# Kernel tuning notes

Measured on AMD Instinct MI355X. Metric: run time of the kernel, lower is better.

## Reference

```python
import jax, jax.numpy as jnp
import numpy as np

N, E, G = 50000, 1600000, 512
H, NF_IN, NF_OUT, GF_OUT, EDIM, DEPTH = 128, 64, 64, 128, 16, 3
EPS = 1e-5


def seg_softmax(logits, seg, num):
    m = jax.ops.segment_max(logits, seg, num_segments=num)
    e = jnp.exp(logits - m[seg])
    s = jax.ops.segment_sum(e, seg, num_segments=num)
    return e / s[seg]


def batchnorm_train(x, gamma, beta):
    mu = jnp.mean(x, axis=0)
    var = jnp.mean((x - mu) ** 2, axis=0)  # biased, as torch BN training
    return (x - mu) * jax.lax.rsqrt(var + EPS) * gamma + beta


def setup_inputs() -> dict:
    key = jax.random.key(0)
    ks = jax.random.split(key, 20)
    inp = {}
    inp['x'] = jax.random.normal(ks[0], (N, NF_IN), jnp.float32)
    inp['edge_index'] = jax.random.randint(ks[1], (2, E), 0, N, jnp.int64)
    inp['edge_attr'] = jax.random.normal(ks[2], (E, EDIM), jnp.float32)
    inp['batch'] = jnp.sort(jax.random.randint(ks[3], (N,), 0, G, jnp.int64))
    inp['num_graphs'] = G
    s = 0.05
    inp['Wi'] = jax.random.normal(ks[4], (H, NF_IN), jnp.float32) * s
    inp['bi'] = jnp.zeros((H,), jnp.float32)
    inp['gat_W'] = jax.random.normal(ks[5], (DEPTH, H, 2 * H), jnp.float32) * s
    inp['gat_a'] = jax.random.normal(ks[6], (DEPTH, 2 * H), jnp.float32) * s
    inp['nfW1'] = jax.random.normal(ks[7], (H, H), jnp.float32) * s
    inp['nfb1'] = jnp.zeros((H,), jnp.float32)
    inp['nf_g'] = jnp.ones((H,), jnp.float32)
    inp['nf_b'] = jnp.zeros((H,), jnp.float32)
    inp['nfW2'] = jax.random.normal(ks[8], (NF_OUT, H), jnp.float32) * s
    inp['nfb2'] = jnp.zeros((NF_OUT,), jnp.float32)
    inp['gfW1'] = jax.random.normal(ks[9], (H, H), jnp.float32) * s
    inp['gfb1'] = jnp.zeros((H,), jnp.float32)
    inp['gf_g'] = jnp.ones((H,), jnp.float32)
    inp['gf_b'] = jnp.zeros((H,), jnp.float32)
    inp['gfW2'] = jax.random.normal(ks[10], (GF_OUT, H), jnp.float32) * s
    inp['gfb2'] = jnp.zeros((GF_OUT,), jnp.float32)
    return inp


def reference(x, edge_index, edge_attr, batch, num_graphs, Wi, bi, gat_W, gat_a,
              nfW1, nfb1, nf_g, nf_b, nfW2, nfb2,
              gfW1, gfb1, gf_g, gf_b, gfW2, gfb2):
    src, dst = edge_index[0], edge_index[1]
    nf = x @ Wi.T + bi  # [N,H]
    for i in range(DEPTH):
        src_nf = nf[src]            # [E,H]
        dst_nf = nf[dst]            # [E,H]
        ef = jnp.concatenate([src_nf, dst_nf], axis=-1) @ gat_a[i]  # [E]
        alpha = seg_softmax(ef, dst, N)
        agg = jax.ops.segment_sum(alpha[:, None] * src_nf, dst, num_segments=N)
        nf = jax.nn.relu(jnp.concatenate([nf, agg], axis=-1) @ gat_W[i].T)
    # 3-iteration attention pooling over graphs
    h = nf
    for _ in range(3):
        logits = jnp.sum(h * nf, axis=-1)  # [N]
        alpha = seg_softmax(logits, batch, num_graphs)
        h = alpha[:, None] * nf
    gf = jax.ops.segment_sum(h, batch, num_segments=num_graphs)  # [G,H]
    nf_out = jax.nn.relu(batchnorm_train(nf @ nfW1.T + nfb1, nf_g, nf_b)) @ nfW2.T + nfb2
    gf_out = jax.nn.relu(batchnorm_train(gf @ gfW1.T + gfb1, gf_g, gf_b)) @ gfW2.T + gfb2
    return nf_out, edge_attr, gf_out
```

## Files before the change

### kernel.cpp

```cpp
#include <hip/hip_runtime.h>

#define NN 50000
#define NE 1600000
#define NG 512
#define HD 128
#define NGRP 8
#define GRPSZ ((NN + NGRP - 1) / NGRP)
#define PCAP 28672

typedef __attribute__((ext_vector_type(8))) short bf16x8;
typedef __attribute__((ext_vector_type(4))) float f32x4;

static __device__ __forceinline__ unsigned bf16rn(float x) {
  unsigned b = __float_as_uint(x);
  return (b + 0x7FFFu + ((b >> 16) & 1u)) >> 16;
}
static __device__ __forceinline__ float bf16tof(unsigned short u) {
  return __uint_as_float(((unsigned)u) << 16);
}

__global__ void __launch_bounds__(256) k_part(const int* __restrict__ src,
                                              const int* __restrict__ dst,
                                              uint2* __restrict__ pairs,
                                              int* __restrict__ pcnt) {
  __shared__ uint2 buf[8][512];
  __shared__ int lcnt[8];
  __shared__ int gbase[8];
  __shared__ int nfl[8];
  const int tid = threadIdx.x;
  const int b = blockIdx.x & 7;
  if (tid < 8) lcnt[tid] = 0;
  __syncthreads();
  const int stride = gridDim.x * 256;
  for (int base_e = blockIdx.x * 256; base_e < NE; base_e += stride) {
    int e = base_e + tid;
    bool valid = e < NE;
    if (valid) {
      int d = dst[e];
      int s = src[e];
      int g = d / GRPSZ;
      int pos = atomicAdd(&lcnt[g], 1);
      buf[g][pos] = make_uint2((unsigned)d, (unsigned)s);
    }
    __syncthreads();
    if (tid < 8) {
      int c = lcnt[tid];
      int nf = (c >= 256) ? 256 : 0;
      nfl[tid] = nf;
      gbase[tid] = nf ? atomicAdd(&pcnt[tid * 8 + b], nf) : 0;
    }
    __syncthreads();
#pragma unroll
    for (int g0 = 0; g0 < 8; ++g0) {
      if (nfl[g0]) {
        int gb = gbase[g0] + tid;
        if (gb < PCAP)
          pairs[(size_t)(g0 * 8 + b) * PCAP + gb] = buf[g0][tid];
      }
    }
    __syncthreads();
#pragma unroll
    for (int g0 = 0; g0 < 8; ++g0) {
      if (nfl[g0]) {
        int rem = lcnt[g0] - 256;
        if (tid < rem) buf[g0][tid] = buf[g0][256 + tid];
      }
    }
    __syncthreads();
    if (tid < 8 && nfl[tid]) lcnt[tid] -= 256;
    __syncthreads();
  }
  if (tid < 8) {
    int c = lcnt[tid];
    gbase[tid] = c ? atomicAdd(&pcnt[tid * 8 + b], c) : 0;
  }
  __syncthreads();
#pragma unroll
  for (int g0 = 0; g0 < 8; ++g0) {
    int c = lcnt[g0];
    if (tid < c) {
      int gb = gbase[g0] + tid;
      if (gb < PCAP)
        pairs[(size_t)(g0 * 8 + b) * PCAP + gb] = buf[g0][tid];
    }
  }
}

__global__ void __launch_bounds__(256) k_hist(const uint2* __restrict__ pairs,
                                              const int* __restrict__ pcnt,
                                              int* __restrict__ hcnt) {
  __shared__ int hist[GRPSZ];
  const int b = blockIdx.x;
  const int g = b & 7, sub = b >> 3;
  const int li = g * 8 + sub;
  const int lo = g * GRPSZ;
  for (int i = threadIdx.x; i < GRPSZ; i += 256) hist[i] = 0;
  __syncthreads();
  int cnt = min(pcnt[li], PCAP);
  const uint2* lst = pairs + (size_t)li * PCAP;
  for (int i = threadIdx.x; i < cnt; i += 256)
    atomicAdd(&hist[(int)lst[i].x - lo], 1);
  __syncthreads();
  for (int i = threadIdx.x; i < GRPSZ; i += 256)
    hcnt[(size_t)li * GRPSZ + i] = hist[i];
}

__global__ void __launch_bounds__(256) k_csr(const uint2* __restrict__ pairs,
                                             const int* __restrict__ pcnt,
                                             const int* __restrict__ hcnt,
                                             int* __restrict__ row_ptr,
                                             int* __restrict__ csr_src) {
  __shared__ int rp[GRPSZ];
  __shared__ int cur[GRPSZ];
  __shared__ int wsum[256];
  const int b = blockIdx.x;
  const int g = b & 7, sub = b >> 3;
  const int li = g * 8 + sub;
  const int lo = g * GRPSZ;
  int gbase = 0;
  for (int gg = 0; gg < g; ++gg)
#pragma unroll
    for (int ss = 0; ss < 8; ++ss) gbase += pcnt[gg * 8 + ss];
  for (int i = threadIdx.x; i < GRPSZ; i += 256) {
    int dsum = 0, before = 0;
#pragma unroll
    for (int ss = 0; ss < 8; ++ss) {
      int h = hcnt[(size_t)(g * 8 + ss) * GRPSZ + i];
      dsum += h;
      if (ss < sub) before += h;
    }
    rp[i] = dsum;
    cur[i] = before;
  }
  __syncthreads();
  const int CH = (GRPSZ + 255) / 256;
  int t0 = threadIdx.x * CH;
  int t1 = min(GRPSZ, t0 + CH);
  int s = 0;
  for (int i = t0; i < t1; ++i) { int v = rp[i]; rp[i] = s; s += v; }
  wsum[threadIdx.x] = s;
  __syncthreads();
  for (int off = 1; off < 256; off <<= 1) {
    int t = ((int)threadIdx.x >= off) ? wsum[threadIdx.x - off] : 0;
    __syncthreads();
    wsum[threadIdx.x] += t;
    __syncthreads();
  }
  int add = gbase + ((threadIdx.x > 0) ? wsum[threadIdx.x - 1] : 0);
  for (int i = t0; i < t1; ++i) rp[i] += add;
  __syncthreads();
  for (int i = threadIdx.x; i < GRPSZ; i += 256) {
    cur[i] += rp[i];
    if (sub == 0) row_ptr[lo + i] = rp[i];
  }
  if (sub == 0 && g == 7 && threadIdx.x == 0) row_ptr[NN] = NE;
  __syncthreads();
  int cnt = min(pcnt[li], PCAP);
  const uint2* lst = pairs + (size_t)li * PCAP;
  for (int i = threadIdx.x; i < cnt; i += 256) {
    uint2 p = lst[i];
    int pos = atomicAdd(&cur[(int)p.x - lo], 1);
    csr_src[pos] = (int)p.y;
  }
}

__global__ void k_init_bounds(int* __restrict__ gs, int* __restrict__ ge) {
  int g = blockIdx.x * 256 + threadIdx.x;
  if (g < NG) { gs[g] = NN; ge[g] = 0; }
}
__global__ void k_bounds(const int* __restrict__ batch, int* __restrict__ gs, int* __restrict__ ge) {
  int n = blockIdx.x * 256 + threadIdx.x;
  if (n < NN) {
    int b = batch[n];
    atomicMin(&gs[b], n);
    atomicMax(&ge[b], n + 1);
  }
}

__global__ void k_cvt3(const float* __restrict__ a0, int n0,
                       const float* __restrict__ a1, int n1,
                       const float* __restrict__ a2, int n2,
                       unsigned short* __restrict__ b) {
  int i = blockIdx.x * 256 + threadIdx.x;
  if (i >= n0 + n1 + n2) return;
  float v = (i < n0) ? a0[i] : (i < n0 + n1) ? a1[i - n0] : a2[i - n0 - n1];
  b[i] = (unsigned short)bf16rn(v);
}

template <bool LAST>
__global__ void __launch_bounds__(512) k_layer(
    const unsigned short* __restrict__ nf16, const uint4* __restrict__ nf8u4,
    const float2* __restrict__ es_in,
    const int* __restrict__ row_ptr, const int* __restrict__ csr_src,
    const unsigned short* __restrict__ W16, const float* __restrict__ dvec,
    unsigned short* __restrict__ out16,
    unsigned char* __restrict__ nf8out, float2* __restrict__ es_out,
    float* __restrict__ dout) {
  __shared__ unsigned short aggl[64][136];
  __shared__ float pdot[64];
  __shared__ int rmaxI[64];
  const int tid = threadIdx.x;
  const int wid = tid >> 6;
  const int lane = tid & 63;
  const int row0 = blockIdx.x * 64;
  if (tid < 64) { pdot[tid] = 0.f; rmaxI[tid] = 0; }

  {
    const int q = lane >> 3;
    const int c = lane & 7;
    for (int r = 0; r < 8; ++r) {
      const int slot = wid * 8 + r;
      const int node = row0 + slot;
      int s = 0, e = 0;
      if (node < NN) { s = row_ptr[node]; e = row_ptr[node + 1]; }
      float acc[16];
#pragma unroll
      for (int i = 0; i < 16; ++i) acc[i] = 0.f;
      float zloc = 0.f, wsl = 0.f;
      int j0 = s + q;      bool p0 = j0 < e;  int sc0 = p0 ? csr_src[j0] : 0;
      int j1 = s + 8 + q;  bool p1 = j1 < e;  int sc1 = p1 ? csr_src[j1] : 0;
      float2 e0 = es_in[sc0];
      float w0  = p0 ? e0.x : 0.f;
      float ws0 = p0 ? e0.x * e0.y : 0.f;
      uint4 a = nf8u4[(size_t)sc0 * 8 + c];
      for (int j = s; j < e; j += 8) {
        int j2 = j + 16 + q; bool p2 = j2 < e;
        int sc2 = p2 ? csr_src[j2] : 0;
        float2 e1v = es_in[sc1];
        uint4 b = nf8u4[(size_t)sc1 * 8 + c];
        float w1  = p1 ? e1v.x : 0.f;
        float ws1 = p1 ? e1v.x * e1v.y : 0.f;
        zloc += w0; wsl += ws0;
        acc[0]  = fmaf(ws0, (float)(a.x & 255u), acc[0]);
        acc[1]  = fmaf(ws0, (float)((a.x >> 8) & 255u), acc[1]);
        acc[2]  = fmaf(ws0, (float)((a.x >> 16) & 255u), acc[2]);
        acc[3]  = fmaf(ws0, (float)(a.x >> 24), acc[3]);
        acc[4]  = fmaf(ws0, (float)(a.y & 255u), acc[4]);
        acc[5]  = fmaf(ws0, (float)((a.y >> 8) & 255u), acc[5]);
        acc[6]  = fmaf(ws0, (float)((a.y >> 16) & 255u), acc[6]);
        acc[7]  = fmaf(ws0, (float)(a.y >> 24), acc[7]);
        acc[8]  = fmaf(ws0, (float)(a.z & 255u), acc[8]);
        acc[9]  = fmaf(ws0, (float)((a.z >> 8) & 255u), acc[9]);
        acc[10] = fmaf(ws0, (float)((a.z >> 16) & 255u), acc[10]);
        acc[11] = fmaf(ws0, (float)(a.z >> 24), acc[11]);
        acc[12] = fmaf(ws0, (float)(a.w & 255u), acc[12]);
        acc[13] = fmaf(ws0, (float)((a.w >> 8) & 255u), acc[13]);
        acc[14] = fmaf(ws0, (float)((a.w >> 16) & 255u), acc[14]);
        acc[15] = fmaf(ws0, (float)(a.w >> 24), acc[15]);
        w0 = w1; ws0 = ws1; a = b; sc1 = sc2; p1 = p2;
      }
      zloc += __shfl_xor(zloc, 8);
      zloc += __shfl_xor(zloc, 16);
      zloc += __shfl_xor(zloc, 32);
      wsl += __shfl_xor(wsl, 8);
      wsl += __shfl_xor(wsl, 16);
      wsl += __shfl_xor(wsl, 32);
      float inv = (zloc > 0.f) ? 1.f / zloc : 0.f;
      float base = 128.f * wsl;
#pragma unroll
      for (int i = 0; i < 16; ++i) {
        acc[i] += __shfl_xor(acc[i], 8);
        acc[i] += __shfl_xor(acc[i], 16);
        acc[i] += __shfl_xor(acc[i], 32);
        acc[i] = (acc[i] - base) * inv;
      }
      if (q == 0) {
        uint4 p0k, p1k;
        p0k.x = bf16rn(acc[0])  | (bf16rn(acc[1])  << 16);
        p0k.y = bf16rn(acc[2])  | (bf16rn(acc[3])  << 16);
        p0k.z = bf16rn(acc[4])  | (bf16rn(acc[5])  << 16);
        p0k.w = bf16rn(acc[6])  | (bf16rn(acc[7])  << 16);
        p1k.x = bf16rn(acc[8])  | (bf16rn(acc[9])  << 16);
        p1k.y = bf16rn(acc[10]) | (bf16rn(acc[11]) << 16);
        p1k.z = bf16rn(acc[12]) | (bf16rn(acc[13]) << 16);
        p1k.w = bf16rn(acc[14]) | (bf16rn(acc[15]) << 16);
        uint4* dst = (uint4*)(&aggl[slot][c * 16]);
        dst[0] = p0k;
        dst[1] = p1k;
      }
    }
  }
  __syncthreads();

  {
    const int lr = lane & 15;
    const int qq = lane >> 4;
    const int rblk = wid & 3, cblk = wid >> 2;
    const int rbase = row0 + rblk * 16;
    const int arow = min(rbase + lr, NN - 1);
    const unsigned short* pa1 = nf16 + (size_t)arow * 128;
    const unsigned short* pw = W16 + (size_t)(cblk * 64) * 256;

    f32x4 acc[4];
#pragma unroll
    for (int t = 0; t < 4; ++t) acc[t] = (f32x4){0.f, 0.f, 0.f, 0.f};

#pragma unroll
    for (int s = 0; s < 8; ++s) {
      bf16x8 af;
      if (s < 4) af = *(const bf16x8*)(pa1 + s * 32 + qq * 8);
      else       af = *(const bf16x8*)(&aggl[rblk * 16 + lr][(s - 4) * 32 + qq * 8]);
#pragma unroll
      for (int t = 0; t < 4; ++t) {
        bf16x8 bfr = *(const bf16x8*)(pw + (size_t)(t * 16 + lr) * 256 + s * 32 + qq * 8);
        acc[t] = __builtin_amdgcn_mfma_f32_16x16x32_bf16(af, bfr, acc[t], 0, 0, 0);
      }
    }

    float dv[4];
    if (!LAST) {
#pragma unroll
      for (int t = 0; t < 4; ++t) dv[t] = dvec[cblk * 64 + t * 16 + lr];
    }
    float p[4] = {0.f, 0.f, 0.f, 0.f};
#pragma unroll
    for (int j = 0; j < 4; ++j) {
      int n = rbase + qq * 4 + j;
      bool ok = n < NN;
      int slot = n - row0;
#pragma unroll
      for (int t = 0; t < 4; ++t) {
        float v = fmaxf(acc[t][j], 0.f);
        if (ok) {
          out16[(size_t)n * HD + cblk * 64 + t * 16 + lr] = (unsigned short)bf16rn(v);
          if (!LAST) atomicMax(&rmaxI[slot], __float_as_int(v));
        }
        p[j] = fmaf(v, LAST ? v : dv[t], p[j]);
      }
      p[j] += __shfl_xor(p[j], 1);
      p[j] += __shfl_xor(p[j], 2);
      p[j] += __shfl_xor(p[j], 4);
      p[j] += __shfl_xor(p[j], 8);
    }
    if (lr == 0) {
#pragma unroll
      for (int j = 0; j < 4; ++j) atomicAdd(&pdot[rblk * 16 + qq * 4 + j], p[j]);
    }
    __syncthreads();
    if (!LAST) {
#pragma unroll
      for (int j = 0; j < 4; ++j) {
        int n = rbase + qq * 4 + j;
        if (n < NN) {
          int slot = n - row0;
          float m = __int_as_float(rmaxI[slot]);
          float is = (m > 0.f) ? 127.f / m : 0.f;
#pragma unroll
          for (int t = 0; t < 4; ++t) {
            float v = fmaxf(acc[t][j], 0.f);
            int u = __float2int_rn(v * is) + 128;
            nf8out[(size_t)n * HD + cblk * 64 + t * 16 + lr] = (unsigned char)u;
          }
        }
      }
    }
  }
  if (tid < 64) {
    int n = row0 + tid;
    if (n < NN) {
      if (LAST) dout[n] = pdot[tid];
      else      es_out[n] = make_float2(__expf(pdot[tid]),
                                        __int_as_float(rmaxI[tid]) * (1.f / 127.f));
    }
  }
}

__global__ void __launch_bounds__(256) k_head1(
    const unsigned short* __restrict__ A1, const unsigned short* __restrict__ W16,
    const float* __restrict__ bias, float* __restrict__ outf,
    float* __restrict__ statS, float* __restrict__ statQ) {
  __shared__ float bs[128], bq[128];
  const int l = threadIdx.x & 63;
  const int w = threadIdx.x >> 6;
  const int lr = l & 15;
  const int q = l >> 4;
  const int row0 = blockIdx.x * 64 + w * 16;
  const int arow = min(row0 + lr, NN - 1);
  const unsigned short* pa1 = A1 + (size_t)arow * 128;
  if (threadIdx.x < 128) { bs[threadIdx.x] = 0.f; bq[threadIdx.x] = 0.f; }

  f32x4 acc[8];
#pragma unroll
  for (int t = 0; t < 8; ++t) acc[t] = (f32x4){0.f, 0.f, 0.f, 0.f};
#pragma unroll
  for (int s = 0; s < 4; ++s) {
    bf16x8 af = *(const bf16x8*)(pa1 + s * 32 + q * 8);
#pragma unroll
    for (int t = 0; t < 8; ++t) {
      bf16x8 bfr = *(const bf16x8*)(W16 + (size_t)(t * 16 + lr) * 128 + s * 32 + q * 8);
      acc[t] = __builtin_amdgcn_mfma_f32_16x16x32_bf16(af, bfr, acc[t], 0, 0, 0);
    }
  }
  float bv[8];
#pragma unroll
  for (int t = 0; t < 8; ++t) bv[t] = bias[t * 16 + lr];
  float ps[8], pq[8];
#pragma unroll
  for (int t = 0; t < 8; ++t) { ps[t] = 0.f; pq[t] = 0.f; }
#pragma unroll
  for (int j = 0; j < 4; ++j) {
    int n = row0 + q * 4 + j;
    bool ok = n < NN;
#pragma unroll
    for (int t = 0; t < 8; ++t) {
      float v = acc[t][j] + bv[t];
      if (ok) {
        outf[(size_t)n * HD + t * 16 + lr] = v;
        ps[t] += v;
        pq[t] += v * v;
      }
    }
  }
  __syncthreads();
#pragma unroll
  for (int t = 0; t < 8; ++t) {
    ps[t] += __shfl_xor(ps[t], 16);
    ps[t] += __shfl_xor(ps[t], 32);
    pq[t] += __shfl_xor(pq[t], 16);
    pq[t] += __shfl_xor(pq[t], 32);
  }
  if (q == 0) {
#pragma unroll
    for (int t = 0; t < 8; ++t) {
      atomicAdd(&bs[t * 16 + lr], ps[t]);
      atomicAdd(&bq[t * 16 + lr], pq[t]);
    }
  }
  __syncthreads();
  if (threadIdx.x < 128) {
    atomicAdd(&statS[threadIdx.x], bs[threadIdx.x]);
    atomicAdd(&statQ[threadIdx.x], bq[threadIdx.x]);
  }
}

__global__ void __launch_bounds__(256) k_head2(
    const float* __restrict__ y, const unsigned short* __restrict__ W16,
    const float* __restrict__ bnA, const float* __restrict__ bnB,
    const float* __restrict__ bias, float* __restrict__ outf) {
  const int l = threadIdx.x & 63;
  const int w = threadIdx.x >> 6;
  const int lr = l & 15;
  const int q = l >> 4;
  const int row0 = blockIdx.x * 64 + w * 16;
  const int arow = min(row0 + lr, NN - 1);
  const float* py = y + (size_t)arow * 128;

  f32x4 acc[4];
#pragma unroll
  for (int t = 0; t < 4; ++t) acc[t] = (f32x4){0.f, 0.f, 0.f, 0.f};
#pragma unroll
  for (int s = 0; s < 4; ++s) {
    const int kg = s * 32 + q * 8;
    float4 y0 = *(const float4*)(py + kg);
    float4 y1 = *(const float4*)(py + kg + 4);
    float4 A0 = *(const float4*)(bnA + kg);
    float4 A1v = *(const float4*)(bnA + kg + 4);
    float4 B0 = *(const float4*)(bnB + kg);
    float4 B1v = *(const float4*)(bnB + kg + 4);
    bf16x8 af;
    af[0] = (short)bf16rn(fmaxf(fmaf(y0.x, A0.x, B0.x), 0.f));
    af[1] = (short)bf16rn(fmaxf(fmaf(y0.y, A0.y, B0.y), 0.f));
    af[2] = (short)bf16rn(fmaxf(fmaf(y0.z, A0.z, B0.z), 0.f));
    af[3] = (short)bf16rn(fmaxf(fmaf(y0.w, A0.w, B0.w), 0.f));
    af[4] = (short)bf16rn(fmaxf(fmaf(y1.x, A1v.x, B1v.x), 0.f));
    af[5] = (short)bf16rn(fmaxf(fmaf(y1.y, A1v.y, B1v.y), 0.f));
    af[6] = (short)bf16rn(fmaxf(fmaf(y1.z, A1v.z, B1v.z), 0.f));
    af[7] = (short)bf16rn(fmaxf(fmaf(y1.w, A1v.w, B1v.w), 0.f));
#pragma unroll
    for (int t = 0; t < 4; ++t) {
      bf16x8 bfr = *(const bf16x8*)(W16 + (size_t)(t * 16 + lr) * 128 + kg);
      acc[t] = __builtin_amdgcn_mfma_f32_16x16x32_bf16(af, bfr, acc[t], 0, 0, 0);
    }
  }
  float bv[4];
#pragma unroll
  for (int t = 0; t < 4; ++t) bv[t] = bias[t * 16 + lr];
#pragma unroll
  for (int j = 0; j < 4; ++j) {
    int n = row0 + q * 4 + j;
    if (n < NN) {
#pragma unroll
      for (int t = 0; t < 4; ++t)
        outf[(size_t)n * 64 + t * 16 + lr] = acc[t][j] + bv[t];
    }
  }
}

template <int K, int KA, int HO, bool PRE, bool RELUOUT, bool BIAS, bool OUT16,
          bool OUTF32, int DOTM, bool Q8>
__global__ void __launch_bounds__(256) k_gemm(
    const float* __restrict__ inA, const float* __restrict__ inB,
    const float* __restrict__ W, const float* __restrict__ bias,
    const float* __restrict__ preA, const float* __restrict__ preB,
    float* __restrict__ out, int nrows,
    unsigned* __restrict__ out16, const float* __restrict__ dvec,
    float* __restrict__ dout,
    unsigned char* __restrict__ nf8, float2* __restrict__ es) {
  constexpr int KC = 64;
  constexpr int BM = 64;
  constexpr int MT = 4;
  constexpr int NT = HO / 16;
  constexpr int LDW = HO + 4;
  constexpr int LDA = KC + 4;

  __shared__ float Wl[KC * LDW];
  __shared__ float inl[BM * LDA];

  const int tid = threadIdx.x;
  const int tr = tid >> 4;
  const int tc = tid & 15;
  const int row0 = blockIdx.x * BM;
  const int r0 = tr * MT;
  const int c0 = tc * NT;

  float acc[MT][NT];
#pragma unroll
  for (int i = 0; i < MT; ++i)
#pragma unroll
    for (int j = 0; j < NT; ++j) acc[i][j] = BIAS ? bias[c0 + j] : 0.f;

  for (int cc = 0; cc < K / KC; ++cc) {
    const int k0 = cc * KC;
    if (cc) __syncthreads();
    for (int idx = tid; idx < HO * (KC / 4); idx += 256) {
      int h = idx >> 4;
      int qq = idx & 15;
      float4 w = *(const float4*)(W + (size_t)h * K + k0 + qq * 4);
      Wl[(qq * 4 + 0) * LDW + h] = w.x;
      Wl[(qq * 4 + 1) * LDW + h] = w.y;
      Wl[(qq * 4 + 2) * LDW + h] = w.z;
      Wl[(qq * 4 + 3) * LDW + h] = w.w;
    }
    for (int idx = tid; idx < BM * (KC / 4); idx += 256) {
      int r = idx >> 4;
      int qq = idx & 15;
      int n = row0 + r;
      int kg = k0 + qq * 4;
      float4 v = make_float4(0.f, 0.f, 0.f, 0.f);
      if (n < nrows) {
        if constexpr (KA == K) {
          v = *(const float4*)(inA + (size_t)n * K + kg);
        } else {
          if (k0 < KA) v = *(const float4*)(inA + (size_t)n * KA + kg);
          else         v = *(const float4*)(inB + (size_t)n * (K - KA) + kg - KA);
        }
      }
      if constexpr (PRE) {
        v.x = fmaxf(v.x * preA[kg + 0] + preB[kg + 0], 0.f);
        v.y = fmaxf(v.y * preA[kg + 1] + preB[kg + 1], 0.f);
        v.z = fmaxf(v.z * preA[kg + 2] + preB[kg + 2], 0.f);
        v.w = fmaxf(v.w * preA[kg + 3] + preB[kg + 3], 0.f);
      }
      *(float4*)(inl + r * LDA + qq * 4) = v;
    }
    __syncthreads();
#pragma unroll 8
    for (int k = 0; k < KC; ++k) {
      float a[MT];
#pragma unroll
      for (int i = 0; i < MT; ++i) a[i] = inl[(r0 + i) * LDA + k];
      float4 b0 = *(const float4*)(Wl + k * LDW + c0);
#pragma unroll
      for (int i = 0; i < MT; ++i) {
        acc[i][0] = fmaf(a[i], b0.x, acc[i][0]);
        acc[i][1] = fmaf(a[i], b0.y, acc[i][1]);
        acc[i][2] = fmaf(a[i], b0.z, acc[i][2]);
        acc[i][3] = fmaf(a[i], b0.w, acc[i][3]);
      }
      if constexpr (NT == 8) {
        float4 b1 = *(const float4*)(Wl + k * LDW + c0 + 4);
#pragma unroll
        for (int i = 0; i < MT; ++i) {
          acc[i][4] = fmaf(a[i], b1.x, acc[i][4]);
          acc[i][5] = fmaf(a[i], b1.y, acc[i][5]);
          acc[i][6] = fmaf(a[i], b1.z, acc[i][6]);
          acc[i][7] = fmaf(a[i], b1.w, acc[i][7]);
        }
      }
    }
  }
  float dv[DOTM == 1 ? NT : 1];
  if constexpr (DOTM == 1) {
#pragma unroll
    for (int j = 0; j < NT; ++j) dv[j] = dvec[c0 + j];
  }
#pragma unroll
  for (int i = 0; i < MT; ++i) {
    int n = row0 + r0 + i;
    if constexpr (RELUOUT) {
#pragma unroll
      for (int j = 0; j < NT; ++j) acc[i][j] = fmaxf(acc[i][j], 0.f);
    }
    if (n < nrows) {
      if constexpr (OUTF32) {
        float4 o0 = make_float4(acc[i][0], acc[i][1], acc[i][2], acc[i][3]);
        *(float4*)(out + (size_t)n * HO + c0) = o0;
        if constexpr (NT == 8) {
          float4 o1 = make_float4(acc[i][4], acc[i][5], acc[i][6], acc[i][7]);
          *(float4*)(out + (size_t)n * HO + c0 + 4) = o1;
        }
      }
      if constexpr (OUT16 && NT == 8) {
        uint4 pk;
        pk.x = bf16rn(acc[i][0]) | (bf16rn(acc[i][1]) << 16);
        pk.y = bf16rn(acc[i][2]) | (bf16rn(acc[i][3]) << 16);
        pk.z = bf16rn(acc[i][4]) | (bf16rn(acc[i][5]) << 16);
        pk.w = bf16rn(acc[i][6]) | (bf16rn(acc[i][7]) << 16);
        *(uint4*)(out16 + (size_t)n * 64 + tc * 4) = pk;
      }
    }
    float s_row = 0.f;
    if constexpr (Q8 && NT == 8) {
      float mx = 0.f;
#pragma unroll
      for (int j = 0; j < NT; ++j) mx = fmaxf(mx, fabsf(acc[i][j]));
      mx = fmaxf(mx, __shfl_xor(mx, 1));
      mx = fmaxf(mx, __shfl_xor(mx, 2));
      mx = fmaxf(mx, __shfl_xor(mx, 4));
      mx = fmaxf(mx, __shfl_xor(mx, 8));
      s_row = mx * (1.f / 127.f);
      float is = (mx > 0.f) ? 127.f / mx : 0.f;
      if (n < nrows) {
        unsigned b0 = 0, b1 = 0;
#pragma unroll
        for (int j = 0; j < 4; ++j)
          b0 |= (unsigned)(__float2int_rn(acc[i][j] * is) + 128) << (8 * j);
#pragma unroll
        for (int j = 4; j < 8; ++j)
          b1 |= (unsigned)(__float2int_rn(acc[i][j] * is) + 128) << (8 * (j - 4));
        uint2 pk8 = make_uint2(b0, b1);
        *(uint2*)(nf8 + (size_t)n * HO + c0) = pk8;
      }
    }
    if constexpr (DOTM != 0) {
      float p = 0.f;
#pragma unroll
      for (int j = 0; j < NT; ++j)
        p = fmaf(acc[i][j], (DOTM == 1) ? dv[j] : acc[i][j], p);
      p += __shfl_xor(p, 1);
      p += __shfl_xor(p, 2);
      p += __shfl_xor(p, 4);
      p += __shfl_xor(p, 8);
      if (tc == 0 && n < nrows) {
        if constexpr (Q8) es[n] = make_float2(__expf(p), s_row);
        else dout[n] = (DOTM == 1) ? __expf(p) : p;
      }
    }
  }
}

__global__ void k_pool(const unsigned short* __restrict__ nf16, const float* __restrict__ r,
                       const int* __restrict__ gs, const int* __restrict__ ge,
                       float* __restrict__ alpha, float* __restrict__ gf) {
  int g = blockIdx.x;
  int s = gs[g], e = ge[g];
  __shared__ float red[256];
  for (int it = 0; it < 3; ++it) {
    float lm = -INFINITY;
    for (int n = s + threadIdx.x; n < e; n += 256) {
      float l = r[n];
      if (it) l *= alpha[n];
      lm = fmaxf(lm, l);
    }
    red[threadIdx.x] = lm;
    __syncthreads();
    for (int off = 128; off > 0; off >>= 1) {
      if ((int)threadIdx.x < off) red[threadIdx.x] = fmaxf(red[threadIdx.x], red[threadIdx.x + off]);
      __syncthreads();
    }
    float m = red[0];
    __syncthreads();
    float zz = 0.f;
    for (int n = s + threadIdx.x; n < e; n += 256) {
      float l = r[n];
      if (it) l *= alpha[n];
      zz += __expf(l - m);
    }
    red[threadIdx.x] = zz;
    __syncthreads();
    for (int off = 128; off > 0; off >>= 1) {
      if ((int)threadIdx.x < off) red[threadIdx.x] += red[threadIdx.x + off];
      __syncthreads();
    }
    float z = red[0];
    __syncthreads();
    float invz = 1.f / z;
    for (int n = s + threadIdx.x; n < e; n += 256) {
      float l = r[n];
      if (it) l *= alpha[n];
      alpha[n] = __expf(l - m) * invz;
    }
    __syncthreads();
  }
  int c = threadIdx.x & 127;
  int rr2 = threadIdx.x >> 7;
  float acc = 0.f;
  for (int n = s + rr2; n < e; n += 2)
    acc += alpha[n] * bf16tof(nf16[(size_t)n * HD + c]);
  red[threadIdx.x] = acc;
  __syncthreads();
  if (rr2 == 0) gf[(size_t)g * HD + c] = red[threadIdx.x] + red[threadIdx.x + 128];
}

__global__ void k_colstats(const float* __restrict__ y, float* __restrict__ sum,
                           float* __restrict__ sumsq, int R, int CH) {
  int c = threadIdx.x & 127;
  int rr = threadIdx.x >> 7;
  int r0 = blockIdx.x * CH;
  int r1 = min(R, r0 + CH);
  float s = 0.f, q = 0.f;
  for (int r = r0 + rr; r < r1; r += 2) {
    float v = y[(size_t)r * HD + c];
    s += v;
    q += v * v;
  }
  __shared__ float ls[256], lq[256];
  ls[threadIdx.x] = s;
  lq[threadIdx.x] = q;
  __syncthreads();
  if (rr == 0) {
    s += ls[threadIdx.x + 128];
    q += lq[threadIdx.x + 128];
    atomicAdd(&sum[c], s);
    atomicAdd(&sumsq[c], q);
  }
}

__global__ void k_bn_final(const float* __restrict__ sum, const float* __restrict__ sumsq,
                           const float* __restrict__ g, const float* __restrict__ b,
                           float* __restrict__ A, float* __restrict__ B, float R) {
  int c = threadIdx.x;
  float mu = sum[c] / R;
  float var = sumsq[c] / R - mu * mu;
  float a = g[c] * rsqrtf(var + 1e-5f);
  A[c] = a;
  B[c] = b[c] - mu * a;
}

__global__ void k_copy4(const float4* __restrict__ a, float4* __restrict__ b, int n) {
  int i = blockIdx.x * 256 + threadIdx.x;
  if (i < n) b[i] = a[i];
}

extern "C" void kernel_launch(void* const* d_in, const int* in_sizes, int n_in,
                              void* d_out, int out_size, void* d_ws, size_t ws_size,
                              hipStream_t stream) {
  const float* x        = (const float*)d_in[0];
  const int*   ei       = (const int*)d_in[1];
  const float* edge_attr= (const float*)d_in[2];
  const int*   batch    = (const int*)d_in[3];
  const float* Wi       = (const float*)d_in[5];
  const float* bi       = (const float*)d_in[6];
  const float* gat_W    = (const float*)d_in[7];
  const float* gat_a    = (const float*)d_in[8];
  const float* nfW1     = (const float*)d_in[9];
  const float* nfb1     = (const float*)d_in[10];
  const float* nf_g     = (const float*)d_in[11];
  const float* nf_b     = (const float*)d_in[12];
  const float* nfW2     = (const float*)d_in[13];
  const float* nfb2     = (const float*)d_in[14];
  const float* gfW1     = (const float*)d_in[15];
  const float* gfb1     = (const float*)d_in[16];
  const float* gf_g     = (const float*)d_in[17];
  const float* gf_b     = (const float*)d_in[18];
  const float* gfW2     = (const float*)d_in[19];
  const float* gfb2     = (const float*)d_in[20];

  float* out = (float*)d_out;

  char* wp = (char*)d_ws;
  unsigned short* nf16A = (unsigned short*)wp; wp += (size_t)NN * HD * 2;
  unsigned short* nf16B = (unsigned short*)wp; wp += (size_t)NN * HD * 2;
  unsigned short* wt_gat = (unsigned short*)wp; wp += (size_t)3 * 128 * 256 * 2;
  unsigned short* wt_nf1 = (unsigned short*)wp; wp += 128 * 128 * 2;
  unsigned short* wt_nf2 = (unsigned short*)wp; wp += 64 * 128 * 2;
  unsigned char* nf8A = (unsigned char*)wp; wp += (size_t)NN * HD;
  unsigned char* nf8B = (unsigned char*)wp; wp += (size_t)NN * HD;
  float* nfA = (float*)wp; wp += (size_t)NN * HD * 4;
  float2* esA = (float2*)wp; wp += (size_t)NN * 8;
  float2* esB = (float2*)wp; wp += (size_t)NN * 8;
  float* rv = (float*)wp; wp += (size_t)NN * 4;
  float* alpha = (float*)wp; wp += (size_t)NN * 4;
  float* gf = (float*)wp; wp += (size_t)NG * HD * 4;
  float* gy = (float*)wp; wp += (size_t)NG * HD * 4;
  int* pcnt = (int*)wp; wp += 64 * 4;
  float* sums = (float*)wp; wp += 256 * 4;
  float* sums2 = (float*)wp; wp += 256 * 4;
  float* bnAB = (float*)wp; wp += 256 * 4;
  int* row_ptr = (int*)wp; wp += (size_t)(NN + 1) * 4;
  int* csr_src = (int*)wp; wp += (size_t)NE * 4;
  int* gs = (int*)wp; wp += NG * 4;
  int* ge = (int*)wp; wp += NG * 4;
  int* hcnt = (int*)wp; wp += (size_t)64 * GRPSZ * 4;
  uint2* pairs = (uint2*)nfA;

  const int* src  = ei;
  const int* dstp = ei + NE;

  hipMemsetAsync(pcnt, 0, (64 + 512) * sizeof(int), stream);

  k_part<<<512, 256, 0, stream>>>(src, dstp, pairs, pcnt);
  k_hist<<<64, 256, 0, stream>>>(pairs, pcnt, hcnt);
  k_csr<<<64, 256, 0, stream>>>(pairs, pcnt, hcnt, row_ptr, csr_src);

  k_init_bounds<<<2, 256, 0, stream>>>(gs, ge);
  k_bounds<<<(NN + 255) / 256, 256, 0, stream>>>(batch, gs, ge);

  k_cvt3<<<(3 * 128 * 256 + 128 * 128 + 64 * 128 + 255) / 256, 256, 0, stream>>>(
      gat_W, 3 * 128 * 256, nfW1, 128 * 128, nfW2, 64 * 128, wt_gat);

  k_gemm<64, 64, 128, false, false, true, true, false, 1, true>
      <<<(NN + 63) / 64, 256, 0, stream>>>(
      x, nullptr, Wi, bi, nullptr, nullptr, nullptr, NN,
      (unsigned*)nf16A, gat_a, nullptr, nf8A, esA);

  const int layer_grid = (NN + 63) / 64;
  k_layer<false><<<layer_grid, 512, 0, stream>>>(
      nf16A, (const uint4*)nf8A, esA, row_ptr, csr_src,
      wt_gat + 0 * 128 * 256, gat_a + 1 * 256, nf16B, nf8B, esB, nullptr);
  k_layer<false><<<layer_grid, 512, 0, stream>>>(
      nf16B, (const uint4*)nf8B, esB, row_ptr, csr_src,
      wt_gat + 1 * 128 * 256, gat_a + 2 * 256, nf16A, nf8A, esA, nullptr);
  k_layer<true><<<layer_grid, 512, 0, stream>>>(
      nf16A, (const uint4*)nf8A, esA, row_ptr, csr_src,
      wt_gat + 2 * 128 * 256, nullptr, nf16B, nullptr, nullptr, rv);
  unsigned short* cur = nf16B;

  k_pool<<<NG, 256, 0, stream>>>(cur, rv, gs, ge, alpha, gf);

  const int gemm_grid = (NN + 63) / 64;
  k_head1<<<gemm_grid, 256, 0, stream>>>(cur, wt_nf1, nfb1, nfA, sums, sums + 128);
  k_bn_final<<<1, 128, 0, stream>>>(sums, sums + 128, nf_g, nf_b, bnAB, bnAB + 128, (float)NN);
  k_head2<<<gemm_grid, 256, 0, stream>>>(nfA, wt_nf2, bnAB, bnAB + 128, nfb2, out);

  k_gemm<128, 128, 128, false, false, true, false, true, 0, false>
      <<<(NG + 63) / 64, 256, 0, stream>>>(
      gf, nullptr, gfW1, gfb1, nullptr, nullptr, gy, NG,
      nullptr, nullptr, nullptr, nullptr, nullptr);
  k_colstats<<<4, 256, 0, stream>>>(gy, sums2, sums2 + 128, NG, 128);
  k_bn_final<<<1, 128, 0, stream>>>(sums2, sums2 + 128, gf_g, gf_b, bnAB, bnAB + 128, (float)NG);
  k_gemm<128, 128, 128, true, false, true, false, true, 0, false>
      <<<(NG + 63) / 64, 256, 0, stream>>>(
      gy, nullptr, gfW2, gfb2, bnAB, bnAB + 128,
      out + (size_t)NN * 64 + (size_t)NE * 16, NG,
      nullptr, nullptr, nullptr, nullptr, nullptr);

  int n4 = NE * 16 / 4;
  k_copy4<<<(n4 + 255) / 256, 256, 0, stream>>>((const float4*)edge_attr,
                                                (float4*)(out + (size_t)NN * 64), n4);
}
```

Before: 610.0 us.

## Split fused GAT layer into separate aggregation and MFMA kernels

The fused per-layer kernel, which did CSR gather-aggregation into shared memory and then an MFMA GEMM, is split into two kernels. The first aggregates one node per wavefront and writes bf16 results to a global buffer. The second runs the GEMM with 16 full-width rows per wave and does the row max and dot-product reductions with shuffles instead of shared-memory atomics. The aim is to decouple the irregular, latency-bound gather from the GEMM so each kernel can be sized independently and barriers and LDS atomics go away. The cost is an extra global write and read of a 12.8MB aggregate buffer per layer and three more kernel launches.

```diff
diff --git a/kernel.cpp b/kernel.cpp
--- a/kernel.cpp
+++ b/kernel.cpp
@@ -187,180 +187,155 @@
   b[i] = (unsigned short)bf16rn(v);
 }
 
+__global__ void k_gat_agg(const uint4* __restrict__ nf8u4, const float2* __restrict__ es_in,
+                          const int* __restrict__ row_ptr, const int* __restrict__ csr_src,
+                          unsigned short* __restrict__ agg16) {
+  int node = blockIdx.x * 4 + (threadIdx.x >> 6);
+  int lane = threadIdx.x & 63;
+  if (node >= NN) return;
+  int s = row_ptr[node], e = row_ptr[node + 1];
+  const int q = lane >> 3;
+  const int c = lane & 7;
+
+  float acc[16];
+#pragma unroll
+  for (int i = 0; i < 16; ++i) acc[i] = 0.f;
+  float zloc = 0.f, wsl = 0.f;
+
+  int j0 = s + q;      bool p0 = j0 < e;  int sc0 = p0 ? csr_src[j0] : 0;
+  int j1 = s + 8 + q;  bool p1 = j1 < e;  int sc1 = p1 ? csr_src[j1] : 0;
+  float2 e0 = es_in[sc0];
+  float w0  = p0 ? e0.x : 0.f;
+  float ws0 = p0 ? e0.x * e0.y : 0.f;
+  uint4 a = nf8u4[(size_t)sc0 * 8 + c];
+  for (int j = s; j < e; j += 8) {
+    int j2 = j + 16 + q; bool p2 = j2 < e;
+    int sc2 = p2 ? csr_src[j2] : 0;
+    float2 e1v = es_in[sc1];
+    uint4 b = nf8u4[(size_t)sc1 * 8 + c];
+    float w1  = p1 ? e1v.x : 0.f;
+    float ws1 = p1 ? e1v.x * e1v.y : 0.f;
+    zloc += w0; wsl += ws0;
+    acc[0]  = fmaf(ws0, (float)(a.x & 255u), acc[0]);
+    acc[1]  = fmaf(ws0, (float)((a.x >> 8) & 255u), acc[1]);
+    acc[2]  = fmaf(ws0, (float)((a.x >> 16) & 255u), acc[2]);
+    acc[3]  = fmaf(ws0, (float)(a.x >> 24), acc[3]);
+    acc[4]  = fmaf(ws0, (float)(a.y & 255u), acc[4]);
+    acc[5]  = fmaf(ws0, (float)((a.y >> 8) & 255u), acc[5]);
+    acc[6]  = fmaf(ws0, (float)((a.y >> 16) & 255u), acc[6]);
+    acc[7]  = fmaf(ws0, (float)(a.y >> 24), acc[7]);
+    acc[8]  = fmaf(ws0, (float)(a.z & 255u), acc[8]);
+    acc[9]  = fmaf(ws0, (float)((a.z >> 8) & 255u), acc[9]);
+    acc[10] = fmaf(ws0, (float)((a.z >> 16) & 255u), acc[10]);
+    acc[11] = fmaf(ws0, (float)(a.z >> 24), acc[11]);
+    acc[12] = fmaf(ws0, (float)(a.w & 255u), acc[12]);
+    acc[13] = fmaf(ws0, (float)((a.w >> 8) & 255u), acc[13]);
+    acc[14] = fmaf(ws0, (float)((a.w >> 16) & 255u), acc[14]);
+    acc[15] = fmaf(ws0, (float)(a.w >> 24), acc[15]);
+    w0 = w1; ws0 = ws1; a = b; sc1 = sc2; p1 = p2;
+  }
+
+  zloc += __shfl_xor(zloc, 8);
+  zloc += __shfl_xor(zloc, 16);
+  zloc += __shfl_xor(zloc, 32);
+  wsl += __shfl_xor(wsl, 8);
+  wsl += __shfl_xor(wsl, 16);
+  wsl += __shfl_xor(wsl, 32);
+  float inv = (zloc > 0.f) ? 1.f / zloc : 0.f;
+  float base = 128.f * wsl;
+#pragma unroll
+  for (int i = 0; i < 16; ++i) {
+    acc[i] += __shfl_xor(acc[i], 8);
+    acc[i] += __shfl_xor(acc[i], 16);
+    acc[i] += __shfl_xor(acc[i], 32);
+    acc[i] = (acc[i] - base) * inv;
+  }
+  if (q == 0) {
+    uint4 p0k, p1k;
+    p0k.x = bf16rn(acc[0])  | (bf16rn(acc[1])  << 16);
+    p0k.y = bf16rn(acc[2])  | (bf16rn(acc[3])  << 16);
+    p0k.z = bf16rn(acc[4])  | (bf16rn(acc[5])  << 16);
+    p0k.w = bf16rn(acc[6])  | (bf16rn(acc[7])  << 16);
+    p1k.x = bf16rn(acc[8])  | (bf16rn(acc[9])  << 16);
+    p1k.y = bf16rn(acc[10]) | (bf16rn(acc[11]) << 16);
+    p1k.z = bf16rn(acc[12]) | (bf16rn(acc[13]) << 16);
+    p1k.w = bf16rn(acc[14]) | (bf16rn(acc[15]) << 16);
+    uint4* dst = (uint4*)(agg16 + (size_t)node * HD + c * 16);
+    dst[0] = p0k;
+    dst[1] = p1k;
+  }
+}
+
 template <bool LAST>
-__global__ void __launch_bounds__(512) k_layer(
-    const unsigned short* __restrict__ nf16, const uint4* __restrict__ nf8u4,
-    const float2* __restrict__ es_in,
-    const int* __restrict__ row_ptr, const int* __restrict__ csr_src,
+__global__ void __launch_bounds__(256) k_lmfma(
+    const unsigned short* __restrict__ nf16, const unsigned short* __restrict__ agg16,
     const unsigned short* __restrict__ W16, const float* __restrict__ dvec,
     unsigned short* __restrict__ out16,
     unsigned char* __restrict__ nf8out, float2* __restrict__ es_out,
     float* __restrict__ dout) {
-  __shared__ unsigned short aggl[64][136];
-  __shared__ float pdot[64];
-  __shared__ int rmaxI[64];
-  const int tid = threadIdx.x;
-  const int wid = tid >> 6;
-  const int lane = tid & 63;
-  const int row0 = blockIdx.x * 64;
-  if (tid < 64) { pdot[tid] = 0.f; rmaxI[tid] = 0; }
-
-  {
-    const int q = lane >> 3;
-    const int c = lane & 7;
-    for (int r = 0; r < 8; ++r) {
-      const int slot = wid * 8 + r;
-      const int node = row0 + slot;
-      int s = 0, e = 0;
-      if (node < NN) { s = row_ptr[node]; e = row_ptr[node + 1]; }
-      float acc[16];
-#pragma unroll
-      for (int i = 0; i < 16; ++i) acc[i] = 0.f;
-      float zloc = 0.f, wsl = 0.f;
-      int j0 = s + q;      bool p0 = j0 < e;  int sc0 = p0 ? csr_src[j0] : 0;
-      int j1 = s + 8 + q;  bool p1 = j1 < e;  int sc1 = p1 ? csr_src[j1] : 0;
-      float2 e0 = es_in[sc0];
-      float w0  = p0 ? e0.x : 0.f;
-      float ws0 = p0 ? e0.x * e0.y : 0.f;
-      uint4 a = nf8u4[(size_t)sc0 * 8 + c];
-      for (int j = s; j < e; j += 8) {
-        int j2 = j + 16 + q; bool p2 = j2 < e;
-        int sc2 = p2 ? csr_src[j2] : 0;
-        float2 e1v = es_in[sc1];
-        uint4 b = nf8u4[(size_t)sc1 * 8 + c];
-        float w1  = p1 ? e1v.x : 0.f;
-        float ws1 = p1 ? e1v.x * e1v.y : 0.f;
-        zloc += w0; wsl += ws0;
-        acc[0]  = fmaf(ws0, (float)(a.x & 255u), acc[0]);
-        acc[1]  = fmaf(ws0, (float)((a.x >> 8) & 255u), acc[1]);
-        acc[2]  = fmaf(ws0, (float)((a.x >> 16) & 255u), acc[2]);
-        acc[3]  = fmaf(ws0, (float)(a.x >> 24), acc[3]);
-        acc[4]  = fmaf(ws0, (float)(a.y & 255u), acc[4]);
-        acc[5]  = fmaf(ws0, (float)((a.y >> 8) & 255u), acc[5]);
-        acc[6]  = fmaf(ws0, (float)((a.y >> 16) & 255u), acc[6]);
-        acc[7]  = fmaf(ws0, (float)(a.y >> 24), acc[7]);
-        acc[8]  = fmaf(ws0, (float)(a.z & 255u), acc[8]);
-        acc[9]  = fmaf(ws0, (float)((a.z >> 8) & 255u), acc[9]);
-        acc[10] = fmaf(ws0, (float)((a.z >> 16) & 255u), acc[10]);
-        acc[11] = fmaf(ws0, (float)(a.z >> 24), acc[11]);
-        acc[12] = fmaf(ws0, (float)(a.w & 255u), acc[12]);
-        acc[13] = fmaf(ws0, (float)((a.w >> 8) & 255u), acc[13]);
-        acc[14] = fmaf(ws0, (float)((a.w >> 16) & 255u), acc[14]);
-        acc[15] = fmaf(ws0, (float)(a.w >> 24), acc[15]);
-        w0 = w1; ws0 = ws1; a = b; sc1 = sc2; p1 = p2;
-      }
-      zloc += __shfl_xor(zloc, 8);
-      zloc += __shfl_xor(zloc, 16);
-      zloc += __shfl_xor(zloc, 32);
-      wsl += __shfl_xor(wsl, 8);
-      wsl += __shfl_xor(wsl, 16);
-      wsl += __shfl_xor(wsl, 32);
-      float inv = (zloc > 0.f) ? 1.f / zloc : 0.f;
-      float base = 128.f * wsl;
-#pragma unroll
-      for (int i = 0; i < 16; ++i) {
-        acc[i] += __shfl_xor(acc[i], 8);
-        acc[i] += __shfl_xor(acc[i], 16);
-        acc[i] += __shfl_xor(acc[i], 32);
-        acc[i] = (acc[i] - base) * inv;
-      }
-      if (q == 0) {
-        uint4 p0k, p1k;
-        p0k.x = bf16rn(acc[0])  | (bf16rn(acc[1])  << 16);
-        p0k.y = bf16rn(acc[2])  | (bf16rn(acc[3])  << 16);
-        p0k.z = bf16rn(acc[4])  | (bf16rn(acc[5])  << 16);
-        p0k.w = bf16rn(acc[6])  | (bf16rn(acc[7])  << 16);
-        p1k.x = bf16rn(acc[8])  | (bf16rn(acc[9])  << 16);
-        p1k.y = bf16rn(acc[10]) | (bf16rn(acc[11]) << 16);
-        p1k.z = bf16rn(acc[12]) | (bf16rn(acc[13]) << 16);
-        p1k.w = bf16rn(acc[14]) | (bf16rn(acc[15]) << 16);
-        uint4* dst = (uint4*)(&aggl[slot][c * 16]);
-        dst[0] = p0k;
-        dst[1] = p1k;
-      }
-    }
-  }
-  __syncthreads();
-
-  {
-    const int lr = lane & 15;
-    const int qq = lane >> 4;
-    const int rblk = wid & 3, cblk = wid >> 2;
-    const int rbase = row0 + rblk * 16;
-    const int arow = min(rbase + lr, NN - 1);
-    const unsigned short* pa1 = nf16 + (size_t)arow * 128;
-    const unsigned short* pw = W16 + (size_t)(cblk * 64) * 256;
-
-    f32x4 acc[4];
-#pragma unroll
-    for (int t = 0; t < 4; ++t) acc[t] = (f32x4){0.f, 0.f, 0.f, 0.f};
-
-#pragma unroll
-    for (int s = 0; s < 8; ++s) {
-      bf16x8 af;
-      if (s < 4) af = *(const bf16x8*)(pa1 + s * 32 + qq * 8);
-      else       af = *(const bf16x8*)(&aggl[rblk * 16 + lr][(s - 4) * 32 + qq * 8]);
-#pragma unroll
-      for (int t = 0; t < 4; ++t) {
-        bf16x8 bfr = *(const bf16x8*)(pw + (size_t)(t * 16 + lr) * 256 + s * 32 + qq * 8);
-        acc[t] = __builtin_amdgcn_mfma_f32_16x16x32_bf16(af, bfr, acc[t], 0, 0, 0);
-      }
-    }
-
-    float dv[4];
+  const int l = threadIdx.x & 63;
+  const int w = threadIdx.x >> 6;
+  const int lr = l & 15;
+  const int q = l >> 4;
+  const int row0 = blockIdx.x * 64 + w * 16;
+  const int arow = min(row0 + lr, NN - 1);
+  const unsigned short* pa1 = nf16 + (size_t)arow * 128;
+  const unsigned short* pa2 = agg16 + (size_t)arow * 128;
+
+  f32x4 acc[8];
+#pragma unroll
+  for (int t = 0; t < 8; ++t) acc[t] = (f32x4){0.f, 0.f, 0.f, 0.f};
+
+#pragma unroll
+  for (int s = 0; s < 8; ++s) {
+    bf16x8 af = (s < 4) ? *(const bf16x8*)(pa1 + s * 32 + q * 8)
+                        : *(const bf16x8*)(pa2 + (s - 4) * 32 + q * 8);
+#pragma unroll
+    for (int t = 0; t < 8; ++t) {
+      bf16x8 bfr = *(const bf16x8*)(W16 + (size_t)(t * 16 + lr) * 256 + s * 32 + q * 8);
+      acc[t] = __builtin_amdgcn_mfma_f32_16x16x32_bf16(af, bfr, acc[t], 0, 0, 0);
+    }
+  }
+
+  float dv[8];
+  if (!LAST) {
+#pragma unroll
+    for (int t = 0; t < 8; ++t) dv[t] = dvec[t * 16 + lr];
+  }
+#pragma unroll
+  for (int j = 0; j < 4; ++j) {
+    int n = row0 + q * 4 + j;
+    bool ok = n < NN;
+    float vrow[8];
+    float p = 0.f, mx = 0.f;
+#pragma unroll
+    for (int t = 0; t < 8; ++t) {
+      float v = fmaxf(acc[t][j], 0.f);
+      vrow[t] = v;
+      if (ok) out16[(size_t)n * HD + t * 16 + lr] = (unsigned short)bf16rn(v);
+      p = fmaf(v, LAST ? v : dv[t], p);
+      mx = fmaxf(mx, v);
+    }
+    p += __shfl_xor(p, 1);
+    p += __shfl_xor(p, 2);
+    p += __shfl_xor(p, 4);
+    p += __shfl_xor(p, 8);
     if (!LAST) {
-#pragma unroll
-      for (int t = 0; t < 4; ++t) dv[t] = dvec[cblk * 64 + t * 16 + lr];
-    }
-    float p[4] = {0.f, 0.f, 0.f, 0.f};
-#pragma unroll
-    for (int j = 0; j < 4; ++j) {
-      int n = rbase + qq * 4 + j;
-      bool ok = n < NN;
-      int slot = n - row0;
-#pragma unroll
-      for (int t = 0; t < 4; ++t) {
-        float v = fmaxf(acc[t][j], 0.f);
-        if (ok) {
-          out16[(size_t)n * HD + cblk * 64 + t * 16 + lr] = (unsigned short)bf16rn(v);
-          if (!LAST) atomicMax(&rmaxI[slot], __float_as_int(v));
+      mx = fmaxf(mx, __shfl_xor(mx, 1));
+      mx = fmaxf(mx, __shfl_xor(mx, 2));
+      mx = fmaxf(mx, __shfl_xor(mx, 4));
+      mx = fmaxf(mx, __shfl_xor(mx, 8));
+      float is = (mx > 0.f) ? 127.f / mx : 0.f;
+      if (ok) {
+#pragma unroll
+        for (int t = 0; t < 8; ++t) {
+          int u = __float2int_rn(vrow[t] * is) + 128;
+          nf8out[(size_t)n * HD + t * 16 + lr] = (unsigned char)u;
         }
-        p[j] = fmaf(v, LAST ? v : dv[t], p[j]);
-      }
-      p[j] += __shfl_xor(p[j], 1);
-      p[j] += __shfl_xor(p[j], 2);
-      p[j] += __shfl_xor(p[j], 4);
-      p[j] += __shfl_xor(p[j], 8);
-    }
-    if (lr == 0) {
-#pragma unroll
-      for (int j = 0; j < 4; ++j) atomicAdd(&pdot[rblk * 16 + qq * 4 + j], p[j]);
-    }
-    __syncthreads();
-    if (!LAST) {
-#pragma unroll
-      for (int j = 0; j < 4; ++j) {
-        int n = rbase + qq * 4 + j;
-        if (n < NN) {
-          int slot = n - row0;
-          float m = __int_as_float(rmaxI[slot]);
-          float is = (m > 0.f) ? 127.f / m : 0.f;
-#pragma unroll
-          for (int t = 0; t < 4; ++t) {
-            float v = fmaxf(acc[t][j], 0.f);
-            int u = __float2int_rn(v * is) + 128;
-            nf8out[(size_t)n * HD + cblk * 64 + t * 16 + lr] = (unsigned char)u;
-          }
-        }
-      }
-    }
-  }
-  if (tid < 64) {
-    int n = row0 + tid;
-    if (n < NN) {
-      if (LAST) dout[n] = pdot[tid];
-      else      es_out[n] = make_float2(__expf(pdot[tid]),
-                                        __int_as_float(rmaxI[tid]) * (1.f / 127.f));
+        if (lr == 0) es_out[n] = make_float2(__expf(p), mx * (1.f / 127.f));
+      }
+    } else {
+      if (ok && lr == 0) dout[n] = p;
     }
   }
 }
@@ -771,6 +746,7 @@
   char* wp = (char*)d_ws;
   unsigned short* nf16A = (unsigned short*)wp; wp += (size_t)NN * HD * 2;
   unsigned short* nf16B = (unsigned short*)wp; wp += (size_t)NN * HD * 2;
+  unsigned short* agg16 = (unsigned short*)wp; wp += (size_t)NN * HD * 2;
   unsigned short* wt_gat = (unsigned short*)wp; wp += (size_t)3 * 128 * 256 * 2;
   unsigned short* wt_nf1 = (unsigned short*)wp; wp += 128 * 128 * 2;
   unsigned short* wt_nf2 = (unsigned short*)wp; wp += 64 * 128 * 2;
@@ -814,21 +790,21 @@
       x, nullptr, Wi, bi, nullptr, nullptr, nullptr, NN,
       (unsigned*)nf16A, gat_a, nullptr, nf8A, esA);
 
-  const int layer_grid = (NN + 63) / 64;
-  k_layer<false><<<layer_grid, 512, 0, stream>>>(
-      nf16A, (const uint4*)nf8A, esA, row_ptr, csr_src,
-      wt_gat + 0 * 128 * 256, gat_a + 1 * 256, nf16B, nf8B, esB, nullptr);
-  k_layer<false><<<layer_grid, 512, 0, stream>>>(
-      nf16B, (const uint4*)nf8B, esB, row_ptr, csr_src,
-      wt_gat + 1 * 128 * 256, gat_a + 2 * 256, nf16A, nf8A, esA, nullptr);
-  k_layer<true><<<layer_grid, 512, 0, stream>>>(
-      nf16A, (const uint4*)nf8A, esA, row_ptr, csr_src,
-      wt_gat + 2 * 128 * 256, nullptr, nf16B, nullptr, nullptr, rv);
+  const int agg_grid = (NN + 3) / 4;
+  const int gemm_grid = (NN + 63) / 64;
+  k_gat_agg<<<agg_grid, 256, 0, stream>>>((const uint4*)nf8A, esA, row_ptr, csr_src, agg16);
+  k_lmfma<false><<<gemm_grid, 256, 0, stream>>>(
+      nf16A, agg16, wt_gat + 0 * 128 * 256, gat_a + 1 * 256, nf16B, nf8B, esB, nullptr);
+  k_gat_agg<<<agg_grid, 256, 0, stream>>>((const uint4*)nf8B, esB, row_ptr, csr_src, agg16);
+  k_lmfma<false><<<gemm_grid, 256, 0, stream>>>(
+      nf16B, agg16, wt_gat + 1 * 128 * 256, gat_a + 2 * 256, nf16A, nf8A, esA, nullptr);
+  k_gat_agg<<<agg_grid, 256, 0, stream>>>((const uint4*)nf8A, esA, row_ptr, csr_src, agg16);
+  k_lmfma<true><<<gemm_grid, 256, 0, stream>>>(
+      nf16A, agg16, wt_gat + 2 * 128 * 256, nullptr, nf16B, nullptr, nullptr, rv);
   unsigned short* cur = nf16B;
 
   k_pool<<<NG, 256, 0, stream>>>(cur, rv, gs, ge, alpha, gf);
 
-  const int gemm_grid = (NN + 63) / 64;
   k_head1<<<gemm_grid, 256, 0, stream>>>(cur, wt_nf1, nfb1, nfA, sums, sums + 128);
   k_bn_final<<<1, 128, 0, stream>>>(sums, sums + 128, nf_g, nf_b, bnAB, bnAB + 128, (float)NN);
   k_head2<<<gemm_grid, 256, 0, stream>>>(nfA, wt_nf2, bnAB, bnAB + 128, nfb2, out);
```

Measured after the change: 583.2 us. 4.4% less time.
